# Performance work log

Hardware: AMD Instinct MI355X
Metric: run time of the kernel (lower is better)

Reference implementation:

```python
import jax, jax.numpy as jnp
import numpy as np

BLOCK = 16
FP4_LEVELS = jnp.array([0.0, 0.5, 1.0, 1.5, 2.0, 3.0, 4.0, 6.0], dtype=jnp.float32)
FP4_MIDS = jnp.array([0.25, 0.75, 1.25, 1.75, 2.5, 3.5, 5.0], dtype=jnp.float32)
E4M3_MAX = 448.0
FP4_MAX = 6.0


def _fp4_round(v):
    # round-to-nearest onto signed E2M1 grid {0,.5,1,1.5,2,3,4,6}
    a = jnp.minimum(jnp.abs(v), FP4_MAX)
    idx = jnp.searchsorted(FP4_MIDS, a, side='right')
    return jnp.sign(v) * FP4_LEVELS[idx]


def _encode_scale(block_amax, global_amax):
    # two-level NVFP4 scaling: block scale stored as FP8 E4M3 relative to global scale
    g_scale = global_amax / (E4M3_MAX * FP4_MAX)
    s = block_amax / FP4_MAX
    s_q = jnp.clip(s / g_scale, 0.0, E4M3_MAX).astype(jnp.float8_e4m3fn).astype(jnp.float32) * g_scale
    return s_q


def nvfp4_qdq_1d(x, block=BLOCK):
    # blockwise fake-quant along the last dim (activations)
    sh = x.shape
    xb = x.reshape(sh[:-1] + (sh[-1] // block, block))
    g_amax = jnp.max(jnp.abs(x))
    b_amax = jnp.max(jnp.abs(xb), axis=-1, keepdims=True)
    s = _encode_scale(b_amax, g_amax)
    s_safe = jnp.where(s > 0, s, 1.0)
    dq = _fp4_round(xb / s_safe) * s
    return dq.reshape(sh)


def nvfp4_qdq_2d(w, block=BLOCK):
    # (16,16) 2D block fake-quant for the weight [out, in]
    O, I = w.shape
    wb = w.reshape(O // block, block, I // block, block)
    g_amax = jnp.max(jnp.abs(w))
    b_amax = jnp.max(jnp.abs(wb), axis=(1, 3), keepdims=True)
    s = _encode_scale(b_amax, g_amax)
    s_safe = jnp.where(s > 0, s, 1.0)
    dq = _fp4_round(wb / s_safe) * s
    return dq.reshape(O, I)


def setup_inputs() -> dict:
    key = jax.random.key(0)
    kx, kw = jax.random.split(key)
    B, S, D_IN, D_OUT = 4, 2048, 4096, 4096
    x = jax.random.normal(kx, (B, S, D_IN), dtype=jnp.float32)
    weight = jax.random.normal(kw, (D_OUT, D_IN), dtype=jnp.float32) * 0.02
    bias = jnp.zeros((D_OUT,), dtype=jnp.float32)
    return {"x": x, "weight": weight, "bias": bias}


def reference(x, weight, bias):
    x_hat = nvfp4_qdq_1d(x)
    x_ste = x + jax.lax.stop_gradient(x_hat - x)
    w_hat = nvfp4_qdq_2d(weight)
    w_ste = weight + jax.lax.stop_gradient(w_hat - weight)
    y = jnp.einsum('bsi,oi->bso', x_ste, w_ste)
    return y + bias
```

## Files before the change

kernel.cpp:

```cpp
#include <hip/hip_runtime.h>

typedef unsigned short u16;
typedef unsigned int u32;
typedef __bf16 bf16x8 __attribute__((ext_vector_type(8)));
typedef float f32x4 __attribute__((ext_vector_type(4)));


__device__ __forceinline__ float e4m3_rne(float r) {
  if (r < 0.015625f) {
    return rintf(r * 512.0f) * (1.0f / 512.0f);
  }
  u32 u = __float_as_uint(r);
  u32 lsb = (u >> 20) & 1u;
  u += 0x7FFFFu + lsb;
  u &= 0xFFF00000u;
  return __uint_as_float(u);
}

__device__ __forceinline__ float fp4_level(float a, const float* t) {
  return a < t[3] ? (a < t[1] ? (a < t[0] ? 0.0f : 0.5f)
                              : (a < t[2] ? 1.0f : 1.5f))
                  : (a < t[5] ? (a < t[4] ? 2.0f : 3.0f)
                              : (a < t[6] ? 4.0f : 6.0f));
}

__device__ __forceinline__ void gload_lds16(const u16* g, void* l) {
  __builtin_amdgcn_global_load_lds(
      (const __attribute__((address_space(1))) void*)g,
      (__attribute__((address_space(3))) void*)l, 16, 0, 0);
}


__global__ void __launch_bounds__(256) amax_part_kernel(const float4* __restrict__ p,
                                                        int n4, float* __restrict__ part) {
  float m = 0.0f;
  int stride = gridDim.x * 256;
  for (int i = blockIdx.x * 256 + threadIdx.x; i < n4; i += stride) {
    float4 v = p[i];
    m = fmaxf(m, fmaxf(fmaxf(fabsf(v.x), fabsf(v.y)), fmaxf(fabsf(v.z), fabsf(v.w))));
  }
#pragma unroll
  for (int o = 32; o > 0; o >>= 1) m = fmaxf(m, __shfl_xor(m, o));
  __shared__ float red[4];
  int wid = threadIdx.x >> 6, lane = threadIdx.x & 63;
  if (lane == 0) red[wid] = m;
  __syncthreads();
  if (threadIdx.x == 0)
    part[blockIdx.x] = fmaxf(fmaxf(red[0], red[1]), fmaxf(red[2], red[3]));
}

__global__ void __launch_bounds__(256) finalize_kernel(const float* __restrict__ px,
                                                       const float* __restrict__ pw,
                                                       float* __restrict__ scal,
                                                       int nx, int nw) {
  int tid = threadIdx.x;
  float mx = 0.0f, mw = 0.0f;
  for (int i = tid; i < nx; i += 256) mx = fmaxf(mx, px[i]);
  for (int i = tid; i < nw; i += 256) mw = fmaxf(mw, pw[i]);
#pragma unroll
  for (int o = 32; o > 0; o >>= 1) {
    mx = fmaxf(mx, __shfl_xor(mx, o));
    mw = fmaxf(mw, __shfl_xor(mw, o));
  }
  __shared__ float rx[4], rw[4];
  int wid = tid >> 6, lane = tid & 63;
  if (lane == 0) { rx[wid] = mx; rw[wid] = mw; }
  __syncthreads();
  if (tid == 0) {
    scal[0] = fmaxf(fmaxf(rx[0], rx[1]), fmaxf(rx[2], rx[3]));
    scal[1] = fmaxf(fmaxf(rw[0], rw[1]), fmaxf(rw[2], rw[3]));
  }
}


__global__ void __launch_bounds__(256) quant_x_kernel(const float* __restrict__ x,
                                                      const float* __restrict__ scal,
                                                      u16* __restrict__ q, int nblk) {
  int b = blockIdx.x * 256 + threadIdx.x;
  if (b >= nblk) return;
  const float4* px = (const float4*)(x + (size_t)b * 16);
  float4 v[4];
  v[0] = px[0]; v[1] = px[1]; v[2] = px[2]; v[3] = px[3];
  float am = 0.0f;
  const float* vf = (const float*)v;
#pragma unroll
  for (int i = 0; i < 16; ++i) am = fmaxf(am, fabsf(vf[i]));

  float g = scal[0] / 2688.0f;
  float ratio = fminf(fmaxf((am / 6.0f) / g, 0.0f), 448.0f);
  float sq = e4m3_rne(ratio);
  float s = sq * g;
  float ss = s > 0.0f ? s : 1.0f;
  float t[7] = {0.25f * ss, 0.75f * ss, 1.25f * ss, 1.75f * ss,
                2.5f * ss, 3.5f * ss, 5.0f * ss};

  union { u16 h[16]; uint4 v4[2]; } ou;
#pragma unroll
  for (int i = 0; i < 16; ++i) {
    float qv = copysignf(fp4_level(fabsf(vf[i]), t) * sq, vf[i]);
    ou.h[i] = (u16)(__float_as_uint(qv) >> 16);
  }
  uint4* qd = (uint4*)(q + (size_t)b * 16);
  qd[0] = ou.v4[0];
  qd[1] = ou.v4[1];
}


__global__ void __launch_bounds__(256) quant_w_kernel(const float* __restrict__ w,
                                                      const float* __restrict__ scal,
                                                      u16* __restrict__ q, int ntc, int K) {
  int wav = blockIdx.x * 4 + (threadIdx.x >> 6);
  int lane = threadIdx.x & 63;
  int tr = wav / ntc, tc = wav % ntc;
  int r = lane >> 2, c = (lane & 3) * 4;
  size_t off = (size_t)(tr * 16 + r) * K + tc * 16 + c;
  float4 v = *(const float4*)(w + off);
  float am = fmaxf(fmaxf(fabsf(v.x), fabsf(v.y)), fmaxf(fabsf(v.z), fabsf(v.w)));
#pragma unroll
  for (int o = 32; o > 0; o >>= 1) am = fmaxf(am, __shfl_xor(am, o));

  float g = scal[1] / 2688.0f;
  float ratio = fminf(fmaxf((am / 6.0f) / g, 0.0f), 448.0f);
  float sq = e4m3_rne(ratio);
  float s = sq * g;
  float ss = s > 0.0f ? s : 1.0f;
  float t[7] = {0.25f * ss, 0.75f * ss, 1.25f * ss, 1.75f * ss,
                2.5f * ss, 3.5f * ss, 5.0f * ss};

  float vf[4] = {v.x, v.y, v.z, v.w};
  union { u16 h[4]; uint2 v2; } ou;
#pragma unroll
  for (int i = 0; i < 4; ++i) {
    float qv = copysignf(fp4_level(fabsf(vf[i]), t) * sq, vf[i]);
    ou.h[i] = (u16)(__float_as_uint(qv) >> 16);
  }
  *(uint2*)(q + off) = ou.v2;
}


#define BM 256
#define BN 256
#define BK 64

__global__ void __launch_bounds__(512, 2) gemm_kernel(const u16* __restrict__ A,
                                                      const u16* __restrict__ B,
                                                      const float* __restrict__ bias,
                                                      const float* __restrict__ scal,
                                                      float* __restrict__ out,
                                                      int M, int N, int K) {
  extern __shared__ char lds[];
  const int tid = threadIdx.x;
  const int wid = tid >> 6, lane = tid & 63;
  const int fr = lane & 15, fc = lane >> 4;
  const int wm = wid >> 2, wn = wid & 3;
  const int sw = (fr & 7) << 4;

  int nwg = gridDim.x, bid = blockIdx.x;
  int q8 = nwg >> 3, r8 = nwg & 7;
  int xcd = bid & 7, loc = bid >> 3;
  int wg = (xcd < r8 ? xcd * (q8 + 1) : r8 * (q8 + 1) + (xcd - r8) * q8) + loc;
  int ntn = N / BN;
  int tm = wg / ntn, tn = wg % ntn;
  int brow = tm * BM, bcol = tn * BN;

  const int srow = tid >> 3;
  const int scol = ((((tid & 7) << 4) ^ ((srow & 7) << 4)) >> 1);
  const u16* gA = A + (size_t)(brow + srow) * K + scol;
  const int rowB0 = (srow & 31) + (srow >> 5) * 128;
  const u16* gB = B + (size_t)(bcol + rowB0) * K + scol;
  const size_t K64r = (size_t)K * 64;
  const size_t K32r = (size_t)K * 32;
  const int ldsAoff = wid << 10;
  const int ldsBoff = ((wid & 3) << 10) + ((wid >> 2) << 14);

#define STAGE_A1(buf, kt, c) \
  gload_lds16(gA + (size_t)(c) * K64r + (kt), (buf) + (c) * 8192 + ldsAoff)
#define STAGE_B1(buf, kt, c) \
  gload_lds16(gB + (size_t)(c) * K32r + (kt), (buf) + 32768 + (c) * 4096 + ldsBoff)

  const u32 ldsbase = (u32)(uintptr_t)(__attribute__((address_space(3))) char*)lds;
  const u32 cb0 = (u32)((fc << 4) ^ sw);
  const u32 cb1 = cb0 ^ 64u;
  const u32 aB0 = ldsbase + (u32)((wm * 128 + fr) * 128) + cb0;
  const u32 aB1 = ldsbase + (u32)((wm * 128 + fr) * 128) + cb1;
  const u32 bB0 = ldsbase + 32768u + (u32)((wn * 64 + fr) * 128) + cb0;
  const u32 bB1 = ldsbase + 32768u + (u32)((wn * 64 + fr) * 128) + cb1;

#define DSR(dst, ad, off) \
  asm volatile("ds_read_b128 %0, %1 offset:" off : "=v"(dst) : "v"(ad))

#define LOAD_A0() do { \
  DSR(a[0][0], aC0, "0");    DSR(a[0][1], aC1, "0");    \
  DSR(a[1][0], aC0, "2048"); DSR(a[1][1], aC1, "2048"); \
  DSR(a[2][0], aC0, "4096"); DSR(a[2][1], aC1, "4096"); \
  DSR(a[3][0], aC0, "6144"); DSR(a[3][1], aC1, "6144"); } while (0)
#define LOAD_A1() do { \
  DSR(a[0][0], aC0, "8192");  DSR(a[0][1], aC1, "8192");  \
  DSR(a[1][0], aC0, "10240"); DSR(a[1][1], aC1, "10240"); \
  DSR(a[2][0], aC0, "12288"); DSR(a[2][1], aC1, "12288"); \
  DSR(a[3][0], aC0, "14336"); DSR(a[3][1], aC1, "14336"); } while (0)
#define LOAD_B0() do { \
  DSR(b0[0][0], bC0, "0");    DSR(b0[0][1], bC1, "0");    \
  DSR(b0[1][0], bC0, "2048"); DSR(b0[1][1], bC1, "2048"); } while (0)
#define LOAD_B1() do { \
  DSR(b1[0][0], bC0, "4096"); DSR(b1[0][1], bC1, "4096"); \
  DSR(b1[1][0], bC0, "6144"); DSR(b1[1][1], bC1, "6144"); } while (0)

#define MMA(qm, qn, af, bf)                                                  \
  _Pragma("unroll") for (int j_ = 0; j_ < 4; ++j_)                           \
  _Pragma("unroll") for (int n_ = 0; n_ < 2; ++n_)                           \
  _Pragma("unroll") for (int k_ = 0; k_ < 2; ++k_)                           \
    acc[(qm) * 4 + j_][(qn) * 2 + n_] = __builtin_amdgcn_mfma_f32_16x16x32_bf16( \
        af[j_][k_], bf[n_][k_], acc[(qm) * 4 + j_][(qn) * 2 + n_], 0, 0, 0);

#define PHASE_MID()                                          \
  __builtin_amdgcn_s_barrier();                              \
  asm volatile("s_waitcnt lgkmcnt(0)" ::: "memory");         \
  __builtin_amdgcn_sched_barrier(0);                         \
  __builtin_amdgcn_s_setprio(1);
#define PHASE_END()                                          \
  __builtin_amdgcn_s_setprio(0);                             \
  __builtin_amdgcn_s_barrier();                              \
  __builtin_amdgcn_sched_barrier(0);

  f32x4 acc[8][4];
  f32x4 zero = {0.0f, 0.0f, 0.0f, 0.0f};
#pragma unroll
  for (int m = 0; m < 8; ++m)
#pragma unroll
    for (int n = 0; n < 4; ++n) acc[m][n] = zero;

  const int NT = K / BK;

  STAGE_A1(lds, 0, 0); STAGE_A1(lds, 0, 1); STAGE_A1(lds, 0, 2); STAGE_A1(lds, 0, 3);
  STAGE_B1(lds, 0, 0); STAGE_B1(lds, 0, 1); STAGE_B1(lds, 0, 2); STAGE_B1(lds, 0, 3);
  STAGE_A1(lds + 65536, BK, 0); STAGE_A1(lds + 65536, BK, 2);
  STAGE_B1(lds + 65536, BK, 1); STAGE_B1(lds + 65536, BK, 3);
  asm volatile("s_waitcnt vmcnt(4)" ::: "memory");
  __builtin_amdgcn_s_barrier();

  bf16x8 a[4][2], b0[2][2], b1[2][2];
  int cur = 0;
  for (int t = 0; t < NT; ++t) {
    const u32 bo = (u32)(cur << 16);
    const u32 aC0 = aB0 + bo, aC1 = aB1 + bo;
    const u32 bC0 = bB0 + bo, bC1 = bB1 + bo;
    char* bq = lds + (cur ^ 1) * 65536;
    char* bp = lds + cur * 65536;
    const int kt1 = (t + 1) * BK, kt2 = (t + 2) * BK;
    const int st1 = (t + 1 < NT), st2 = (t + 2 < NT);

    LOAD_A0();
    LOAD_B0();
    if (st1) { STAGE_A1(bq, kt1, 1); STAGE_A1(bq, kt1, 3); }
    PHASE_MID();
    MMA(0, 0, a, b0);
    PHASE_END();

    LOAD_B1();
    if (st1) { STAGE_B1(bq, kt1, 0); STAGE_B1(bq, kt1, 2); }
    PHASE_MID();
    MMA(0, 1, a, b1);
    __builtin_amdgcn_s_setprio(0);
    asm volatile("s_waitcnt vmcnt(4)" ::: "memory");
    __builtin_amdgcn_s_barrier();
    __builtin_amdgcn_sched_barrier(0);

    LOAD_A1();
    if (st2) { STAGE_A1(bp, kt2, 0); STAGE_A1(bp, kt2, 2); }
    PHASE_MID();
    MMA(1, 1, a, b1);
    PHASE_END();

    if (st2) { STAGE_B1(bp, kt2, 1); STAGE_B1(bp, kt2, 3); }
    __builtin_amdgcn_s_setprio(1);
    MMA(1, 0, a, b0);
    __builtin_amdgcn_s_setprio(0);
    if (st2) asm volatile("s_waitcnt vmcnt(4)" ::: "memory");
    else     asm volatile("s_waitcnt vmcnt(0)" ::: "memory");
    __builtin_amdgcn_s_barrier();
    __builtin_amdgcn_sched_barrier(0);
    cur ^= 1;
  }

  float gs = (scal[0] / 2688.0f) * (scal[1] / 2688.0f);
#pragma unroll
  for (int n = 0; n < 4; ++n) {
    int col = bcol + wn * 64 + n * 16 + fr;
    float bv = bias[col];
#pragma unroll
    for (int m = 0; m < 8; ++m) {
      int row0 = brow + wm * 128 + m * 16 + (fc << 2);
      f32x4 v = acc[m][n];
#pragma unroll
      for (int j = 0; j < 4; ++j)
        out[(size_t)(row0 + j) * N + col] = v[j] * gs + bv;
    }
  }
}


extern "C" void kernel_launch(void* const* d_in, const int* in_sizes, int n_in,
                              void* d_out, int out_size, void* d_ws, size_t ws_size,
                              hipStream_t stream) {
  const float* x = (const float*)d_in[0];
  const float* w = (const float*)d_in[1];
  const float* bias = (const float*)d_in[2];
  float* out = (float*)d_out;

  const int DOUT = in_sizes[2];
  const int K = in_sizes[1] / DOUT;
  const int M = in_sizes[0] / K;
  const int N = DOUT;

  float* scal = (float*)d_ws;
  float* px = (float*)((char*)d_ws + 256);
  float* pw = px + 1024;
  u16* qw = (u16*)((char*)d_ws + 8192);
  u16* qx = (u16*)((char*)d_ws + 8192 + (size_t)N * K * 2);

  amax_part_kernel<<<1024, 256, 0, stream>>>((const float4*)x, (M * K) / 4, px);
  amax_part_kernel<<<512, 256, 0, stream>>>((const float4*)w, (N * K) / 4, pw);
  finalize_kernel<<<1, 256, 0, stream>>>(px, pw, scal, 1024, 512);

  int nblk = (M * K) / 16;
  quant_x_kernel<<<(nblk + 255) / 256, 256, 0, stream>>>(x, scal, qx, nblk);

  int ntiles = (N / 16) * (K / 16);
  quant_w_kernel<<<ntiles / 4, 256, 0, stream>>>(w, scal, qw, K / 16, K);

  gemm_kernel<<<(M / BM) * (N / BN), 512, 131072, stream>>>(qx, qw, bias, scal, out,
                                                            M, N, K);
}
```

Before: 335.2 us.

## Shrink GEMM tile to 128x128 with simpler double-buffered pipeline

Reduces the GEMM block tile from 256x256 to 128x128, halves LDS use per block to 64KB, and raises the occupancy hint to 4 blocks per CU. The four-phase interleaved load/MMA schedule is replaced by a single load-all, then MMA-all loop per K step, each wave computing a 64x32 sub-tile. This targets higher occupancy and simpler code, but each loaded byte is reused half as much, so global and LDS traffic per FLOP doubles, and the finer-grained overlap of LDS reads with MFMA is lost.

```diff
diff --git a/kernel.cpp b/kernel.cpp
--- a/kernel.cpp
+++ b/kernel.cpp
@@ -138,11 +138,11 @@
 }
 
 
-#define BM 256
-#define BN 256
+#define BM 128
+#define BN 128
 #define BK 64
 
-__global__ void __launch_bounds__(512, 2) gemm_kernel(const u16* __restrict__ A,
+__global__ void __launch_bounds__(512, 4) gemm_kernel(const u16* __restrict__ A,
                                                       const u16* __restrict__ B,
                                                       const float* __restrict__ bias,
                                                       const float* __restrict__ scal,
@@ -166,118 +166,78 @@
   const int srow = tid >> 3;
   const int scol = ((((tid & 7) << 4) ^ ((srow & 7) << 4)) >> 1);
   const u16* gA = A + (size_t)(brow + srow) * K + scol;
-  const int rowB0 = (srow & 31) + (srow >> 5) * 128;
-  const u16* gB = B + (size_t)(bcol + rowB0) * K + scol;
+  const u16* gB = B + (size_t)(bcol + srow) * K + scol;
   const size_t K64r = (size_t)K * 64;
-  const size_t K32r = (size_t)K * 32;
-  const int ldsAoff = wid << 10;
-  const int ldsBoff = ((wid & 3) << 10) + ((wid >> 2) << 14);
-
-#define STAGE_A1(buf, kt, c) \
-  gload_lds16(gA + (size_t)(c) * K64r + (kt), (buf) + (c) * 8192 + ldsAoff)
-#define STAGE_B1(buf, kt, c) \
-  gload_lds16(gB + (size_t)(c) * K32r + (kt), (buf) + 32768 + (c) * 4096 + ldsBoff)
+
+#define STAGE_AB(buf, kt) do {                                               \
+    gload_lds16(gA + (kt), (buf) + tid * 16);                                \
+    gload_lds16(gA + K64r + (kt), (buf) + 8192 + tid * 16);                  \
+    gload_lds16(gB + (kt), (buf) + 16384 + tid * 16);                        \
+    gload_lds16(gB + K64r + (kt), (buf) + 24576 + tid * 16);                 \
+  } while (0)
 
   const u32 ldsbase = (u32)(uintptr_t)(__attribute__((address_space(3))) char*)lds;
   const u32 cb0 = (u32)((fc << 4) ^ sw);
   const u32 cb1 = cb0 ^ 64u;
-  const u32 aB0 = ldsbase + (u32)((wm * 128 + fr) * 128) + cb0;
-  const u32 aB1 = ldsbase + (u32)((wm * 128 + fr) * 128) + cb1;
-  const u32 bB0 = ldsbase + 32768u + (u32)((wn * 64 + fr) * 128) + cb0;
-  const u32 bB1 = ldsbase + 32768u + (u32)((wn * 64 + fr) * 128) + cb1;
+  const u32 aB0 = ldsbase + (u32)((wm * 64 + fr) * 128) + cb0;
+  const u32 aB1 = ldsbase + (u32)((wm * 64 + fr) * 128) + cb1;
+  const u32 bB0 = ldsbase + 16384u + (u32)((wn * 32 + fr) * 128) + cb0;
+  const u32 bB1 = ldsbase + 16384u + (u32)((wn * 32 + fr) * 128) + cb1;
 
 #define DSR(dst, ad, off) \
   asm volatile("ds_read_b128 %0, %1 offset:" off : "=v"(dst) : "v"(ad))
 
-#define LOAD_A0() do { \
+#define LOAD_AB() do { \
   DSR(a[0][0], aC0, "0");    DSR(a[0][1], aC1, "0");    \
   DSR(a[1][0], aC0, "2048"); DSR(a[1][1], aC1, "2048"); \
   DSR(a[2][0], aC0, "4096"); DSR(a[2][1], aC1, "4096"); \
-  DSR(a[3][0], aC0, "6144"); DSR(a[3][1], aC1, "6144"); } while (0)
-#define LOAD_A1() do { \
-  DSR(a[0][0], aC0, "8192");  DSR(a[0][1], aC1, "8192");  \
-  DSR(a[1][0], aC0, "10240"); DSR(a[1][1], aC1, "10240"); \
-  DSR(a[2][0], aC0, "12288"); DSR(a[2][1], aC1, "12288"); \
-  DSR(a[3][0], aC0, "14336"); DSR(a[3][1], aC1, "14336"); } while (0)
-#define LOAD_B0() do { \
-  DSR(b0[0][0], bC0, "0");    DSR(b0[0][1], bC1, "0");    \
-  DSR(b0[1][0], bC0, "2048"); DSR(b0[1][1], bC1, "2048"); } while (0)
-#define LOAD_B1() do { \
-  DSR(b1[0][0], bC0, "4096"); DSR(b1[0][1], bC1, "4096"); \
-  DSR(b1[1][0], bC0, "6144"); DSR(b1[1][1], bC1, "6144"); } while (0)
-
-#define MMA(qm, qn, af, bf)                                                  \
-  _Pragma("unroll") for (int j_ = 0; j_ < 4; ++j_)                           \
+  DSR(a[3][0], aC0, "6144"); DSR(a[3][1], aC1, "6144"); \
+  DSR(b[0][0], bC0, "0");    DSR(b[0][1], bC1, "0");    \
+  DSR(b[1][0], bC0, "2048"); DSR(b[1][1], bC1, "2048"); } while (0)
+
+#define MMA16() \
+  _Pragma("unroll") for (int m_ = 0; m_ < 4; ++m_)                           \
   _Pragma("unroll") for (int n_ = 0; n_ < 2; ++n_)                           \
   _Pragma("unroll") for (int k_ = 0; k_ < 2; ++k_)                           \
-    acc[(qm) * 4 + j_][(qn) * 2 + n_] = __builtin_amdgcn_mfma_f32_16x16x32_bf16( \
-        af[j_][k_], bf[n_][k_], acc[(qm) * 4 + j_][(qn) * 2 + n_], 0, 0, 0);
-
-#define PHASE_MID()                                          \
-  __builtin_amdgcn_s_barrier();                              \
-  asm volatile("s_waitcnt lgkmcnt(0)" ::: "memory");         \
-  __builtin_amdgcn_sched_barrier(0);                         \
-  __builtin_amdgcn_s_setprio(1);
-#define PHASE_END()                                          \
-  __builtin_amdgcn_s_setprio(0);                             \
-  __builtin_amdgcn_s_barrier();                              \
-  __builtin_amdgcn_sched_barrier(0);
-
-  f32x4 acc[8][4];
+    acc[m_][n_] = __builtin_amdgcn_mfma_f32_16x16x32_bf16(                   \
+        a[m_][k_], b[n_][k_], acc[m_][n_], 0, 0, 0);
+
+  f32x4 acc[4][2];
   f32x4 zero = {0.0f, 0.0f, 0.0f, 0.0f};
 #pragma unroll
-  for (int m = 0; m < 8; ++m)
-#pragma unroll
-    for (int n = 0; n < 4; ++n) acc[m][n] = zero;
+  for (int m = 0; m < 4; ++m)
+#pragma unroll
+    for (int n = 0; n < 2; ++n) acc[m][n] = zero;
 
   const int NT = K / BK;
 
-  STAGE_A1(lds, 0, 0); STAGE_A1(lds, 0, 1); STAGE_A1(lds, 0, 2); STAGE_A1(lds, 0, 3);
-  STAGE_B1(lds, 0, 0); STAGE_B1(lds, 0, 1); STAGE_B1(lds, 0, 2); STAGE_B1(lds, 0, 3);
-  STAGE_A1(lds + 65536, BK, 0); STAGE_A1(lds + 65536, BK, 2);
-  STAGE_B1(lds + 65536, BK, 1); STAGE_B1(lds + 65536, BK, 3);
+  STAGE_AB(lds, 0);
+  STAGE_AB(lds + 32768, BK);
   asm volatile("s_waitcnt vmcnt(4)" ::: "memory");
   __builtin_amdgcn_s_barrier();
 
-  bf16x8 a[4][2], b0[2][2], b1[2][2];
+  bf16x8 a[4][2], b[2][2];
   int cur = 0;
   for (int t = 0; t < NT; ++t) {
-    const u32 bo = (u32)(cur << 16);
+    const u32 bo = (u32)(cur << 15);
     const u32 aC0 = aB0 + bo, aC1 = aB1 + bo;
     const u32 bC0 = bB0 + bo, bC1 = bB1 + bo;
-    char* bq = lds + (cur ^ 1) * 65536;
-    char* bp = lds + cur * 65536;
-    const int kt1 = (t + 1) * BK, kt2 = (t + 2) * BK;
-    const int st1 = (t + 1 < NT), st2 = (t + 2 < NT);
-
-    LOAD_A0();
-    LOAD_B0();
-    if (st1) { STAGE_A1(bq, kt1, 1); STAGE_A1(bq, kt1, 3); }
-    PHASE_MID();
-    MMA(0, 0, a, b0);
-    PHASE_END();
-
-    LOAD_B1();
-    if (st1) { STAGE_B1(bq, kt1, 0); STAGE_B1(bq, kt1, 2); }
-    PHASE_MID();
-    MMA(0, 1, a, b1);
+    char* bp = lds + cur * 32768;
+
+    LOAD_AB();
+    asm volatile("s_waitcnt lgkmcnt(0)" ::: "memory");
+    __builtin_amdgcn_sched_barrier(0);
+    __builtin_amdgcn_s_barrier();
+
+    if (t + 2 < NT) STAGE_AB(bp, (t + 2) * BK);
+    __builtin_amdgcn_sched_barrier(0);
+
+    __builtin_amdgcn_s_setprio(1);
+    MMA16();
     __builtin_amdgcn_s_setprio(0);
-    asm volatile("s_waitcnt vmcnt(4)" ::: "memory");
-    __builtin_amdgcn_s_barrier();
-    __builtin_amdgcn_sched_barrier(0);
-
-    LOAD_A1();
-    if (st2) { STAGE_A1(bp, kt2, 0); STAGE_A1(bp, kt2, 2); }
-    PHASE_MID();
-    MMA(1, 1, a, b1);
-    PHASE_END();
-
-    if (st2) { STAGE_B1(bp, kt2, 1); STAGE_B1(bp, kt2, 3); }
-    __builtin_amdgcn_s_setprio(1);
-    MMA(1, 0, a, b0);
-    __builtin_amdgcn_s_setprio(0);
-    if (st2) asm volatile("s_waitcnt vmcnt(4)" ::: "memory");
-    else     asm volatile("s_waitcnt vmcnt(0)" ::: "memory");
+
+    if (t + 2 < NT) asm volatile("s_waitcnt vmcnt(4)" ::: "memory");
+    else            asm volatile("s_waitcnt vmcnt(0)" ::: "memory");
     __builtin_amdgcn_s_barrier();
     __builtin_amdgcn_sched_barrier(0);
     cur ^= 1;
@@ -285,12 +245,12 @@
 
   float gs = (scal[0] / 2688.0f) * (scal[1] / 2688.0f);
 #pragma unroll
-  for (int n = 0; n < 4; ++n) {
-    int col = bcol + wn * 64 + n * 16 + fr;
+  for (int n = 0; n < 2; ++n) {
+    int col = bcol + wn * 32 + n * 16 + fr;
     float bv = bias[col];
 #pragma unroll
-    for (int m = 0; m < 8; ++m) {
-      int row0 = brow + wm * 128 + m * 16 + (fc << 2);
+    for (int m = 0; m < 4; ++m) {
+      int row0 = brow + wm * 64 + m * 16 + (fc << 2);
       f32x4 v = acc[m][n];
 #pragma unroll
       for (int j = 0; j < 4; ++j)
@@ -329,6 +289,6 @@
   int ntiles = (N / 16) * (K / 16);
   quant_w_kernel<<<ntiles / 4, 256, 0, stream>>>(w, scal, qw, K / 16, K);
 
-  gemm_kernel<<<(M / BM) * (N / BN), 512, 131072, stream>>>(qx, qw, bias, scal, out,
-                                                            M, N, K);
-}
+  gemm_kernel<<<(M / BM) * (N / BN), 512, 65536, stream>>>(qx, qw, bias, scal, out,
+                                                           M, N, K);
+}
```

Result: slower. 440.6 us (+31.4%).

## Replace 8-wave ping-pong schedule with simpler double-buffered single-barrier loop

Applied to the files above, without the earlier changes.

Replaces the four-phase barrier-synchronised pipeline, which prefetched two K-tiles ahead with partial stages, with a plain double buffer. Each iteration stages the entire next A and B tile in two groups of four loads, then waits vmcnt(0) once at the end. It also changes the B staging layout to contiguous rows and adds a second A register set so both halves of the tile are held at once. The aim is fewer barriers and less phase sync overhead, at the cost of a shallower prefetch depth, a full memory drain every iteration, and more register pressure.

```diff
diff --git a/kernel.cpp b/kernel.cpp
--- a/kernel.cpp
+++ b/kernel.cpp
@@ -166,17 +166,22 @@
   const int srow = tid >> 3;
   const int scol = ((((tid & 7) << 4) ^ ((srow & 7) << 4)) >> 1);
   const u16* gA = A + (size_t)(brow + srow) * K + scol;
-  const int rowB0 = (srow & 31) + (srow >> 5) * 128;
-  const u16* gB = B + (size_t)(bcol + rowB0) * K + scol;
+  const u16* gB = B + (size_t)(bcol + srow) * K + scol;
   const size_t K64r = (size_t)K * 64;
-  const size_t K32r = (size_t)K * 32;
-  const int ldsAoff = wid << 10;
-  const int ldsBoff = ((wid & 3) << 10) + ((wid >> 2) << 14);
-
-#define STAGE_A1(buf, kt, c) \
-  gload_lds16(gA + (size_t)(c) * K64r + (kt), (buf) + (c) * 8192 + ldsAoff)
-#define STAGE_B1(buf, kt, c) \
-  gload_lds16(gB + (size_t)(c) * K32r + (kt), (buf) + 32768 + (c) * 4096 + ldsBoff)
+  const int ldsOff = wid << 10;
+
+#define STAGE_A4(buf, kt) do {                                                \
+    gload_lds16(gA + (kt), (buf) + ldsOff);                                   \
+    gload_lds16(gA + K64r + (kt), (buf) + 8192 + ldsOff);                     \
+    gload_lds16(gA + 2 * K64r + (kt), (buf) + 16384 + ldsOff);                \
+    gload_lds16(gA + 3 * K64r + (kt), (buf) + 24576 + ldsOff);                \
+  } while (0)
+#define STAGE_B4(buf, kt) do {                                                \
+    gload_lds16(gB + (kt), (buf) + 32768 + ldsOff);                           \
+    gload_lds16(gB + K64r + (kt), (buf) + 40960 + ldsOff);                    \
+    gload_lds16(gB + 2 * K64r + (kt), (buf) + 49152 + ldsOff);                \
+    gload_lds16(gB + 3 * K64r + (kt), (buf) + 57344 + ldsOff);                \
+  } while (0)
 
   const u32 ldsbase = (u32)(uintptr_t)(__attribute__((address_space(3))) char*)lds;
   const u32 cb0 = (u32)((fc << 4) ^ sw);
@@ -189,16 +194,16 @@
 #define DSR(dst, ad, off) \
   asm volatile("ds_read_b128 %0, %1 offset:" off : "=v"(dst) : "v"(ad))
 
-#define LOAD_A0() do { \
-  DSR(a[0][0], aC0, "0");    DSR(a[0][1], aC1, "0");    \
-  DSR(a[1][0], aC0, "2048"); DSR(a[1][1], aC1, "2048"); \
-  DSR(a[2][0], aC0, "4096"); DSR(a[2][1], aC1, "4096"); \
-  DSR(a[3][0], aC0, "6144"); DSR(a[3][1], aC1, "6144"); } while (0)
-#define LOAD_A1() do { \
-  DSR(a[0][0], aC0, "8192");  DSR(a[0][1], aC1, "8192");  \
-  DSR(a[1][0], aC0, "10240"); DSR(a[1][1], aC1, "10240"); \
-  DSR(a[2][0], aC0, "12288"); DSR(a[2][1], aC1, "12288"); \
-  DSR(a[3][0], aC0, "14336"); DSR(a[3][1], aC1, "14336"); } while (0)
+#define LOAD_A0(dst) do { \
+  DSR(dst[0][0], aC0, "0");    DSR(dst[0][1], aC1, "0");    \
+  DSR(dst[1][0], aC0, "2048"); DSR(dst[1][1], aC1, "2048"); \
+  DSR(dst[2][0], aC0, "4096"); DSR(dst[2][1], aC1, "4096"); \
+  DSR(dst[3][0], aC0, "6144"); DSR(dst[3][1], aC1, "6144"); } while (0)
+#define LOAD_A1(dst) do { \
+  DSR(dst[0][0], aC0, "8192");  DSR(dst[0][1], aC1, "8192");  \
+  DSR(dst[1][0], aC0, "10240"); DSR(dst[1][1], aC1, "10240"); \
+  DSR(dst[2][0], aC0, "12288"); DSR(dst[2][1], aC1, "12288"); \
+  DSR(dst[3][0], aC0, "14336"); DSR(dst[3][1], aC1, "14336"); } while (0)
 #define LOAD_B0() do { \
   DSR(b0[0][0], bC0, "0");    DSR(b0[0][1], bC1, "0");    \
   DSR(b0[1][0], bC0, "2048"); DSR(b0[1][1], bC1, "2048"); } while (0)
@@ -213,16 +218,6 @@
     acc[(qm) * 4 + j_][(qn) * 2 + n_] = __builtin_amdgcn_mfma_f32_16x16x32_bf16( \
         af[j_][k_], bf[n_][k_], acc[(qm) * 4 + j_][(qn) * 2 + n_], 0, 0, 0);
 
-#define PHASE_MID()                                          \
-  __builtin_amdgcn_s_barrier();                              \
-  asm volatile("s_waitcnt lgkmcnt(0)" ::: "memory");         \
-  __builtin_amdgcn_sched_barrier(0);                         \
-  __builtin_amdgcn_s_setprio(1);
-#define PHASE_END()                                          \
-  __builtin_amdgcn_s_setprio(0);                             \
-  __builtin_amdgcn_s_barrier();                              \
-  __builtin_amdgcn_sched_barrier(0);
-
   f32x4 acc[8][4];
   f32x4 zero = {0.0f, 0.0f, 0.0f, 0.0f};
 #pragma unroll
@@ -232,52 +227,44 @@
 
   const int NT = K / BK;
 
-  STAGE_A1(lds, 0, 0); STAGE_A1(lds, 0, 1); STAGE_A1(lds, 0, 2); STAGE_A1(lds, 0, 3);
-  STAGE_B1(lds, 0, 0); STAGE_B1(lds, 0, 1); STAGE_B1(lds, 0, 2); STAGE_B1(lds, 0, 3);
-  STAGE_A1(lds + 65536, BK, 0); STAGE_A1(lds + 65536, BK, 2);
-  STAGE_B1(lds + 65536, BK, 1); STAGE_B1(lds + 65536, BK, 3);
-  asm volatile("s_waitcnt vmcnt(4)" ::: "memory");
+  STAGE_A4(lds, 0);
+  STAGE_B4(lds, 0);
+  asm volatile("s_waitcnt vmcnt(0)" ::: "memory");
   __builtin_amdgcn_s_barrier();
 
-  bf16x8 a[4][2], b0[2][2], b1[2][2];
+  bf16x8 a[4][2], a2[4][2], b0[2][2], b1[2][2];
   int cur = 0;
   for (int t = 0; t < NT; ++t) {
     const u32 bo = (u32)(cur << 16);
     const u32 aC0 = aB0 + bo, aC1 = aB1 + bo;
     const u32 bC0 = bB0 + bo, bC1 = bB1 + bo;
     char* bq = lds + (cur ^ 1) * 65536;
-    char* bp = lds + cur * 65536;
-    const int kt1 = (t + 1) * BK, kt2 = (t + 2) * BK;
-    const int st1 = (t + 1 < NT), st2 = (t + 2 < NT);
-
-    LOAD_A0();
+    const int kt1 = (t + 1) * BK;
+    const int st1 = (t + 1 < NT);
+
+    LOAD_A0(a);
     LOAD_B0();
-    if (st1) { STAGE_A1(bq, kt1, 1); STAGE_A1(bq, kt1, 3); }
-    PHASE_MID();
+    LOAD_B1();
+    if (st1) STAGE_A4(bq, kt1);
+    asm volatile("s_waitcnt lgkmcnt(0)" ::: "memory");
+    __builtin_amdgcn_sched_barrier(0);
+    __builtin_amdgcn_s_setprio(1);
     MMA(0, 0, a, b0);
-    PHASE_END();
-
-    LOAD_B1();
-    if (st1) { STAGE_B1(bq, kt1, 0); STAGE_B1(bq, kt1, 2); }
-    PHASE_MID();
     MMA(0, 1, a, b1);
     __builtin_amdgcn_s_setprio(0);
-    asm volatile("s_waitcnt vmcnt(4)" ::: "memory");
-    __builtin_amdgcn_s_barrier();
-    __builtin_amdgcn_sched_barrier(0);
-
-    LOAD_A1();
-    if (st2) { STAGE_A1(bp, kt2, 0); STAGE_A1(bp, kt2, 2); }
-    PHASE_MID();
-    MMA(1, 1, a, b1);
-    PHASE_END();
-
-    if (st2) { STAGE_B1(bp, kt2, 1); STAGE_B1(bp, kt2, 3); }
+    __builtin_amdgcn_sched_barrier(0);
+
+    LOAD_A1(a2);
+    if (st1) STAGE_B4(bq, kt1);
+    asm volatile("s_waitcnt lgkmcnt(0)" ::: "memory");
+    __builtin_amdgcn_sched_barrier(0);
     __builtin_amdgcn_s_setprio(1);
-    MMA(1, 0, a, b0);
+    MMA(1, 1, a2, b1);
+    MMA(1, 0, a2, b0);
     __builtin_amdgcn_s_setprio(0);
-    if (st2) asm volatile("s_waitcnt vmcnt(4)" ::: "memory");
-    else     asm volatile("s_waitcnt vmcnt(0)" ::: "memory");
+    __builtin_amdgcn_sched_barrier(0);
+
+    asm volatile("s_waitcnt vmcnt(0)" ::: "memory");
     __builtin_amdgcn_s_barrier();
     __builtin_amdgcn_sched_barrier(0);
     cur ^= 1;
```

Measured after the change: 334.2 us. No clear change (-0.3%).
